# Optimization experiments

Measured on AMD Instinct MI355X. Metric: run time of the kernel, lower is better.

Reference implementation:

```python
import jax, jax.numpy as jnp
import numpy as np

N_HEADS = 16
ROPE_BASE = 10000.0


def _rope_tables(T, head_dim, dtype):
    d2 = head_dim // 2
    inv_freq = 1.0 / (ROPE_BASE ** (jnp.arange(0, head_dim, 2, dtype=jnp.float32) / head_dim))
    t = jnp.arange(T, dtype=jnp.float32)
    freqs = jnp.outer(t, inv_freq)  # [T, d2]
    cos = jnp.cos(freqs)[None, :, None, :].astype(dtype)  # [1,T,1,d2]
    sin = jnp.sin(freqs)[None, :, None, :].astype(dtype)
    return cos, sin


def _apply_rotary(x, cos, sin):
    # x: [B,T,H,D]; rotate halves
    d = x.shape[-1] // 2
    x1, x2 = x[..., :d], x[..., d:]
    return jnp.concatenate([x1 * cos + x2 * sin, -x1 * sin + x2 * cos], axis=-1)


def setup_inputs() -> dict:
    key = jax.random.key(0)
    k1, k2, k3 = jax.random.split(key, 3)
    B, T, C = 2, 2048, 1024
    x = jax.random.normal(k1, (B, T, C), dtype=jnp.float32)
    w_attn = jax.random.normal(k2, (3 * C, C), dtype=jnp.float32) * (1.0 / np.sqrt(C))
    w_proj = jax.random.normal(k3, (C, C), dtype=jnp.float32) * (1.0 / np.sqrt(C))
    return {"x": x, "w_attn": w_attn, "w_proj": w_proj}


def reference(x, w_attn, w_proj):
    B, T, C = x.shape
    H = N_HEADS
    D = C // H
    qkv = jnp.einsum('btc,fc->btf', x, w_attn)  # [B,T,3C]
    q, k, v = jnp.split(qkv, 3, axis=2)
    q = q.reshape(B, T, H, D)
    k = k.reshape(B, T, H, D)
    v = v.reshape(B, T, H, D)
    cos, sin = _rope_tables(T, D, x.dtype)
    q = _apply_rotary(q, cos, sin)
    k = _apply_rotary(k, cos, sin)
    # causal SDPA, scale 1/sqrt(D)
    scale = 1.0 / np.sqrt(D)
    scores = jnp.einsum('bqhd,bkhd->bhqk', q, k) * scale
    causal = jnp.tril(jnp.ones((T, T), dtype=bool))
    scores = jnp.where(causal[None, None], scores, jnp.finfo(scores.dtype).min)
    attn = jax.nn.softmax(scores, axis=-1)
    y = jnp.einsum('bhqk,bkhd->bqhd', attn, v).reshape(B, T, C)
    return jnp.einsum('btc,oc->bto', y, w_proj)
```

## Files before the change

### kernel.cpp

```cpp
#include <hip/hip_runtime.h>
#include <math.h>

typedef __bf16 bf16x8 __attribute__((ext_vector_type(8)));
typedef float f32x4 __attribute__((ext_vector_type(4)));

__device__ __forceinline__ unsigned f2bf(float f) {
    union { float f; unsigned u; } v; v.f = f;
    return (v.u + 0x7FFFu + ((v.u >> 16) & 1u)) >> 16;
}

__device__ __forceinline__ void gload16(const ushort* g, ushort* l) {
    __builtin_amdgcn_global_load_lds(
        (const __attribute__((address_space(1))) void*)g,
        (__attribute__((address_space(3))) void*)l, 16, 0, 0);
}

__device__ __forceinline__ bool src_is_fp32(const unsigned* s) {
    int sane = 0;
#pragma unroll
    for (int i = 0; i < 64; ++i) {
        unsigned lo = s[i] & 0xFFFFu;
        unsigned e = (lo >> 7) & 0xFF;
        if (lo == 0u || (e >= 100u && e <= 140u)) sane++;
    }
    return sane < 48;
}

__global__ __launch_bounds__(256) void tobf16_all_kernel(
    const unsigned* __restrict__ s0, const unsigned* __restrict__ s1,
    const unsigned* __restrict__ s2,
    ushort* __restrict__ d0, ushort* __restrict__ d1, ushort* __restrict__ d2) {
    const int bx = blockIdx.x;
    const unsigned* src;
    ushort* dst;
    int lb;
    if (bx < 2048)      { src = s0; dst = d0; lb = bx; }
    else if (bx < 3584) { src = s1; dst = d1; lb = bx - 2048; }
    else                { src = s2; dst = d2; lb = bx - 3584; }
    const int i = lb * 2048 + threadIdx.x * 8;
    if (src_is_fp32(src)) {
        const float* fs = (const float*)src;
        float4 f0 = *(const float4*)(fs + i);
        float4 f1 = *(const float4*)(fs + i + 4);
        uint4 o;
        o.x = f2bf(f0.x) | (f2bf(f0.y) << 16);
        o.y = f2bf(f0.z) | (f2bf(f0.w) << 16);
        o.z = f2bf(f1.x) | (f2bf(f1.y) << 16);
        o.w = f2bf(f1.z) | (f2bf(f1.w) << 16);
        *(uint4*)(dst + i) = o;
    } else {
        *(uint4*)(dst + i) = *(const uint4*)((const ushort*)src + i);
    }
}

constexpr int GBM = 128, GBN = 128, GBK = 32;

__global__ __launch_bounds__(256) void gemm_qkv_rope_kernel(
    const ushort* __restrict__ A, const ushort* __restrict__ Bmat,
    ushort* __restrict__ qkvh, int K) {
    __shared__ ushort As[GBM * GBK];
    __shared__ ushort Bs[GBN * GBK];

    const int tid  = threadIdx.x;
    const int lane = tid & 63;
    const int wv   = tid >> 6;
    const int wm   = (wv >> 1) * 64;
    const int wn   = (wv & 1) * 64;

    const ushort* Ab = A + (size_t)blockIdx.x * GBM * K;
    const ushort* Bb = Bmat + (size_t)blockIdx.y * GBN * K;

    f32x4 acc[4][4];
#pragma unroll
    for (int i = 0; i < 4; i++)
#pragma unroll
        for (int j = 0; j < 4; j++) acc[i][j] = (f32x4){0.f, 0.f, 0.f, 0.f};

    const int srow = tid >> 2;
    const int scol = (tid & 3) * 8;
    const int fr = lane & 15;
    const int fk = (lane >> 4) * 8;
    ushort* adst = As + wv * 512;
    ushort* bdst = Bs + wv * 512;

    for (int k0 = 0; k0 < K; k0 += GBK) {
        __syncthreads();
        gload16(Ab + (size_t)srow * K + k0 + scol,        adst);
        gload16(Ab + (size_t)(srow + 64) * K + k0 + scol, adst + 2048);
        gload16(Bb + (size_t)srow * K + k0 + scol,        bdst);
        gload16(Bb + (size_t)(srow + 64) * K + k0 + scol, bdst + 2048);
        __syncthreads();

        bf16x8 af[4], bfr[4];
#pragma unroll
        for (int i = 0; i < 4; i++)
            af[i] = *(const bf16x8*)(As + (wm + i * 16 + fr) * GBK + fk);
#pragma unroll
        for (int j = 0; j < 4; j++)
            bfr[j] = *(const bf16x8*)(Bs + (wn + j * 16 + fr) * GBK + fk);
#pragma unroll
        for (int i = 0; i < 4; i++)
#pragma unroll
            for (int j = 0; j < 4; j++)
                acc[i][j] = __builtin_amdgcn_mfma_f32_16x16x32_bf16(af[i], bfr[j], acc[i][j], 0, 0, 0);
    }

    const int crow0 = (lane >> 4) * 4;
    const int col0  = blockIdx.y * GBN + wn;
    const int which = col0 >> 10;
    const int hh    = (col0 >> 6) & 15;
    ushort* outp = qkvh + (size_t)which * 4194304 + (size_t)hh * 131072;

    if (which < 2) {
        const float inva = exp2f((float)fr * -0.41524101186f);
        const float invb = exp2f((float)(fr + 16) * -0.41524101186f);
        const float qs = (which == 0) ? 0.125f : 1.0f;
#pragma unroll
        for (int i = 0; i < 4; i++)
#pragma unroll
            for (int r = 0; r < 4; r++) {
                int row = blockIdx.x * GBM + wm + i * 16 + crow0 + r;
                int t = row & 2047;
                size_t ob = ((size_t)(row >> 11)) * 2097152 + (size_t)t * 64;
                float sa, ca, sb, cb;
                __sincosf((float)t * inva, &sa, &ca);
                __sincosf((float)t * invb, &sb, &cb);
                float q0 = acc[i][0][r], q1 = acc[i][1][r];
                float q2 = acc[i][2][r], q3 = acc[i][3][r];
                float n0 = (q0 * ca + q2 * sa) * qs;
                float n1 = (q1 * cb + q3 * sb) * qs;
                float n2 = (q2 * ca - q0 * sa) * qs;
                float n3 = (q3 * cb - q1 * sb) * qs;
                outp[ob + fr]      = (ushort)f2bf(n0);
                outp[ob + 16 + fr] = (ushort)f2bf(n1);
                outp[ob + 32 + fr] = (ushort)f2bf(n2);
                outp[ob + 48 + fr] = (ushort)f2bf(n3);
            }
    } else {
#pragma unroll
        for (int i = 0; i < 4; i++)
#pragma unroll
            for (int r = 0; r < 4; r++) {
                int row = blockIdx.x * GBM + wm + i * 16 + crow0 + r;
                int t = row & 2047;
                size_t ob = ((size_t)(row >> 11)) * 2097152 + (size_t)t * 64;
#pragma unroll
                for (int j = 0; j < 4; j++)
                    outp[ob + j * 16 + fr] = (ushort)f2bf(acc[i][j][r]);
            }
    }
}

__global__ __launch_bounds__(256) void gemm_bt_kernel(
    const ushort* __restrict__ A, const ushort* __restrict__ Bmat,
    float* __restrict__ C, int M, int N, int K) {
    __shared__ ushort As[GBM * GBK];
    __shared__ ushort Bs[GBN * GBK];

    const int tid  = threadIdx.x;
    const int lane = tid & 63;
    const int wv   = tid >> 6;
    const int wm   = (wv >> 1) * 64;
    const int wn   = (wv & 1) * 64;

    const ushort* Ab = A + (size_t)blockIdx.x * GBM * K;
    const ushort* Bb = Bmat + (size_t)blockIdx.y * GBN * K;

    f32x4 acc[4][4];
#pragma unroll
    for (int i = 0; i < 4; i++)
#pragma unroll
        for (int j = 0; j < 4; j++) acc[i][j] = (f32x4){0.f, 0.f, 0.f, 0.f};

    const int srow = tid >> 2;
    const int scol = (tid & 3) * 8;
    const int fr = lane & 15;
    const int fk = (lane >> 4) * 8;
    ushort* adst = As + wv * 512;
    ushort* bdst = Bs + wv * 512;

    for (int k0 = 0; k0 < K; k0 += GBK) {
        __syncthreads();
        gload16(Ab + (size_t)srow * K + k0 + scol,        adst);
        gload16(Ab + (size_t)(srow + 64) * K + k0 + scol, adst + 2048);
        gload16(Bb + (size_t)srow * K + k0 + scol,        bdst);
        gload16(Bb + (size_t)(srow + 64) * K + k0 + scol, bdst + 2048);
        __syncthreads();

        bf16x8 af[4], bfr[4];
#pragma unroll
        for (int i = 0; i < 4; i++)
            af[i] = *(const bf16x8*)(As + (wm + i * 16 + fr) * GBK + fk);
#pragma unroll
        for (int j = 0; j < 4; j++)
            bfr[j] = *(const bf16x8*)(Bs + (wn + j * 16 + fr) * GBK + fk);
#pragma unroll
        for (int i = 0; i < 4; i++)
#pragma unroll
            for (int j = 0; j < 4; j++)
                acc[i][j] = __builtin_amdgcn_mfma_f32_16x16x32_bf16(af[i], bfr[j], acc[i][j], 0, 0, 0);
    }

    const int crow0 = (lane >> 4) * 4;
#pragma unroll
    for (int i = 0; i < 4; i++)
#pragma unroll
        for (int j = 0; j < 4; j++)
#pragma unroll
            for (int r = 0; r < 4; r++) {
                int row = blockIdx.x * GBM + wm + i * 16 + crow0 + r;
                int col = blockIdx.y * GBN + wn + j * 16 + fr;
                C[(size_t)row * N + col] = acc[i][j][r];
            }
}

#define NEG_BIG (-1e30f)
constexpr int LPK = 72;
constexpr int LPV = 136;

__global__ __launch_bounds__(256) void attn_kernel(const ushort* __restrict__ qkvh,
                                                   ushort* __restrict__ y) {
    __shared__ ushort Ks[128 * LPK];
    __shared__ ushort Vt[64 * LPV];
    __shared__ ushort Ps[4][16 * LPV];

    const int tid  = threadIdx.x;
    const int lane = tid & 63;
    const int wv   = tid >> 6;
    const int pid  = blockIdx.x;
    const int bh   = blockIdx.y;
    const int b    = bh >> 4, h = bh & 15;

    const ushort* qp = qkvh + (size_t)b * 2097152 + (size_t)h * 131072;
    const ushort* kp = qp + 4194304;
    const ushort* vp = qp + 8388608;

    const int fr = lane & 15;
    const int fq = lane >> 4;
    const int fk = fq * 8;

    const int srow = tid >> 1;
    const int scol = (tid & 1) * 32;
    const int vkey = tid & 127;
    const int vd0  = (tid >> 7) * 32;

#pragma unroll 1
    for (int seg = 0; seg < 2; ++seg) {
        const int qb = seg ? (31 - pid) : pid;
        const int nIt = (qb + 2) >> 1;

        const int qrow = qb * 64 + wv * 16 + fr;
        bf16x8 qf0 = *(const bf16x8*)(qp + (size_t)qrow * 64 + fk);
        bf16x8 qf1 = *(const bf16x8*)(qp + (size_t)qrow * 64 + 32 + fk);

        f32x4 o[4];
        o[0] = o[1] = o[2] = o[3] = (f32x4){0.f, 0.f, 0.f, 0.f};
        float lacc[4] = {0.f, 0.f, 0.f, 0.f};

        uint4 kr0, kr1, kr2, kr3, vr0, vr1, vr2, vr3;
        {
            const ushort* sk = kp + (size_t)srow * 64 + scol;
            kr0 = *(const uint4*)(sk);
            kr1 = *(const uint4*)(sk + 8);
            kr2 = *(const uint4*)(sk + 16);
            kr3 = *(const uint4*)(sk + 24);
            const ushort* sv = vp + (size_t)vkey * 64 + vd0;
            vr0 = *(const uint4*)(sv);
            vr1 = *(const uint4*)(sv + 8);
            vr2 = *(const uint4*)(sv + 16);
            vr3 = *(const uint4*)(sv + 24);
        }

#pragma unroll 1
        for (int it = 0; it < nIt; ++it) {
            const int k0 = it * 128;
            __syncthreads();
            *(uint4*)(Ks + srow * LPK + scol)      = kr0;
            *(uint4*)(Ks + srow * LPK + scol + 8)  = kr1;
            *(uint4*)(Ks + srow * LPK + scol + 16) = kr2;
            *(uint4*)(Ks + srow * LPK + scol + 24) = kr3;
            {
                unsigned w[16] = {vr0.x, vr0.y, vr0.z, vr0.w, vr1.x, vr1.y, vr1.z, vr1.w,
                                  vr2.x, vr2.y, vr2.z, vr2.w, vr3.x, vr3.y, vr3.z, vr3.w};
#pragma unroll
                for (int jj = 0; jj < 16; ++jj) {
                    Vt[(vd0 + 2 * jj)     * LPV + vkey] = (ushort)(w[jj] & 0xFFFFu);
                    Vt[(vd0 + 2 * jj + 1) * LPV + vkey] = (ushort)(w[jj] >> 16);
                }
            }
            __syncthreads();
            if (it + 1 < nIt) {
                const ushort* sk = kp + (size_t)(k0 + 128 + srow) * 64 + scol;
                kr0 = *(const uint4*)(sk);
                kr1 = *(const uint4*)(sk + 8);
                kr2 = *(const uint4*)(sk + 16);
                kr3 = *(const uint4*)(sk + 24);
                const ushort* sv = vp + (size_t)(k0 + 128 + vkey) * 64 + vd0;
                vr0 = *(const uint4*)(sv);
                vr1 = *(const uint4*)(sv + 8);
                vr2 = *(const uint4*)(sv + 16);
                vr3 = *(const uint4*)(sv + 24);
            }

            f32x4 s[8];
#pragma unroll
            for (int j = 0; j < 8; ++j) {
                bf16x8 kf0 = *(const bf16x8*)(Ks + (j * 16 + fr) * LPK + fk);
                bf16x8 kf1 = *(const bf16x8*)(Ks + (j * 16 + fr) * LPK + 32 + fk);
                f32x4 z = (f32x4){0.f, 0.f, 0.f, 0.f};
                z = __builtin_amdgcn_mfma_f32_16x16x32_bf16(qf0, kf0, z, 0, 0, 0);
                z = __builtin_amdgcn_mfma_f32_16x16x32_bf16(qf1, kf1, z, 0, 0, 0);
                s[j] = z;
            }
            if (it + 1 < nIt) {
#pragma unroll
                for (int j = 0; j < 8; ++j)
#pragma unroll
                    for (int r = 0; r < 4; ++r) {
                        float p = __expf(s[j][r]);
                        s[j][r] = p;
                        lacc[r] += p;
                    }
            } else {
                const int rowg = qb * 64 + wv * 16 + fq * 4;
#pragma unroll
                for (int j = 0; j < 8; ++j)
#pragma unroll
                    for (int r = 0; r < 4; ++r) {
                        float v = s[j][r];
                        if ((k0 + j * 16 + fr) > (rowg + r)) v = NEG_BIG;
                        float p = __expf(v);
                        s[j][r] = p;
                        lacc[r] += p;
                    }
            }

            ushort* pw = Ps[wv];
#pragma unroll
            for (int j = 0; j < 8; ++j)
#pragma unroll
                for (int r = 0; r < 4; ++r)
                    pw[(fq * 4 + r) * LPV + j * 16 + fr] = (ushort)f2bf(s[j][r]);
            __asm__ volatile("" ::: "memory");

#pragma unroll
            for (int kk = 0; kk < 4; ++kk) {
                bf16x8 pf = *(const bf16x8*)(pw + fr * LPV + kk * 32 + fk);
#pragma unroll
                for (int j = 0; j < 4; ++j) {
                    bf16x8 vf = *(const bf16x8*)(Vt + (j * 16 + fr) * LPV + kk * 32 + fk);
                    o[j] = __builtin_amdgcn_mfma_f32_16x16x32_bf16(pf, vf, o[j], 0, 0, 0);
                }
            }
        }

#pragma unroll
        for (int msk = 1; msk < 16; msk <<= 1)
#pragma unroll
            for (int r = 0; r < 4; ++r)
                lacc[r] += __shfl_xor(lacc[r], msk, 64);
#pragma unroll
        for (int j = 0; j < 4; ++j)
#pragma unroll
            for (int r = 0; r < 4; ++r) {
                int row = qb * 64 + wv * 16 + fq * 4 + r;
                y[((size_t)b * 2048 + row) * 1024 + h * 64 + j * 16 + fr] =
                    (ushort)f2bf(o[j][r] / lacc[r]);
            }
    }
}

extern "C" void kernel_launch(void* const* d_in, const int* in_sizes, int n_in,
                              void* d_out, int out_size, void* d_ws, size_t ws_size,
                              hipStream_t stream) {
    const int nx = in_sizes[0];
    const int na = in_sizes[1];
    const int np = in_sizes[2];

    ushort* qkvh = (ushort*)d_ws;
    ushort* yb   = qkvh + (size_t)3 * 4194304;
    ushort* xb   = yb + (size_t)4096 * 1024;
    ushort* wab  = xb + nx;
    ushort* wpb  = wab + na;
    size_t need = ((size_t)3 * 4194304 + (size_t)4096 * 1024 + nx + na + np) * 2;
    if (ws_size < need) return;

    tobf16_all_kernel<<<dim3(4096), 256, 0, stream>>>(
        (const unsigned*)d_in[0], (const unsigned*)d_in[1], (const unsigned*)d_in[2],
        xb, wab, wpb);

    gemm_qkv_rope_kernel<<<dim3(32, 24), 256, 0, stream>>>(xb, wab, qkvh, 1024);
    attn_kernel<<<dim3(16, 32), 256, 0, stream>>>(qkvh, yb);
    gemm_bt_kernel<<<dim3(32, 8), 256, 0, stream>>>(yb, wpb, (float*)d_out, 4096, 1024, 1024);
}
```

Baseline: 204.9 us.

## Double-buffer LDS tiles in GEMMs and attention with smaller key blocks

```diff
diff --git a/kernel.cpp b/kernel.cpp
--- a/kernel.cpp
+++ b/kernel.cpp
@@ -58,8 +58,8 @@
 __global__ __launch_bounds__(256) void gemm_qkv_rope_kernel(
     const ushort* __restrict__ A, const ushort* __restrict__ Bmat,
     ushort* __restrict__ qkvh, int K) {
-    __shared__ ushort As[GBM * GBK];
-    __shared__ ushort Bs[GBN * GBK];
+    __shared__ ushort As[2][GBM * GBK];
+    __shared__ ushort Bs[2][GBN * GBK];
 
     const int tid  = threadIdx.x;
     const int lane = tid & 63;
@@ -80,24 +80,31 @@
     const int scol = (tid & 3) * 8;
     const int fr = lane & 15;
     const int fk = (lane >> 4) * 8;
-    ushort* adst = As + wv * 512;
-    ushort* bdst = Bs + wv * 512;
-
-    for (int k0 = 0; k0 < K; k0 += GBK) {
+    const int nK = K >> 5;
+
+    gload16(Ab + (size_t)srow * K + scol,        As[0] + wv * 512);
+    gload16(Ab + (size_t)(srow + 64) * K + scol, As[0] + wv * 512 + 2048);
+    gload16(Bb + (size_t)srow * K + scol,        Bs[0] + wv * 512);
+    gload16(Bb + (size_t)(srow + 64) * K + scol, Bs[0] + wv * 512 + 2048);
+
+#pragma unroll 1
+    for (int it = 0; it < nK; ++it) {
+        const int cur = it & 1;
         __syncthreads();
-        gload16(Ab + (size_t)srow * K + k0 + scol,        adst);
-        gload16(Ab + (size_t)(srow + 64) * K + k0 + scol, adst + 2048);
-        gload16(Bb + (size_t)srow * K + k0 + scol,        bdst);
-        gload16(Bb + (size_t)(srow + 64) * K + k0 + scol, bdst + 2048);
-        __syncthreads();
-
+        if (it + 1 < nK) {
+            const int k0 = (it + 1) << 5, nxt = cur ^ 1;
+            gload16(Ab + (size_t)srow * K + k0 + scol,        As[nxt] + wv * 512);
+            gload16(Ab + (size_t)(srow + 64) * K + k0 + scol, As[nxt] + wv * 512 + 2048);
+            gload16(Bb + (size_t)srow * K + k0 + scol,        Bs[nxt] + wv * 512);
+            gload16(Bb + (size_t)(srow + 64) * K + k0 + scol, Bs[nxt] + wv * 512 + 2048);
+        }
         bf16x8 af[4], bfr[4];
 #pragma unroll
         for (int i = 0; i < 4; i++)
-            af[i] = *(const bf16x8*)(As + (wm + i * 16 + fr) * GBK + fk);
+            af[i] = *(const bf16x8*)(As[cur] + (wm + i * 16 + fr) * GBK + fk);
 #pragma unroll
         for (int j = 0; j < 4; j++)
-            bfr[j] = *(const bf16x8*)(Bs + (wn + j * 16 + fr) * GBK + fk);
+            bfr[j] = *(const bf16x8*)(Bs[cur] + (wn + j * 16 + fr) * GBK + fk);
 #pragma unroll
         for (int i = 0; i < 4; i++)
 #pragma unroll
@@ -154,8 +161,8 @@
 __global__ __launch_bounds__(256) void gemm_bt_kernel(
     const ushort* __restrict__ A, const ushort* __restrict__ Bmat,
     float* __restrict__ C, int M, int N, int K) {
-    __shared__ ushort As[GBM * GBK];
-    __shared__ ushort Bs[GBN * GBK];
+    __shared__ ushort As[2][GBM * GBK];
+    __shared__ ushort Bs[2][GBN * GBK];
 
     const int tid  = threadIdx.x;
     const int lane = tid & 63;
@@ -176,24 +183,31 @@
     const int scol = (tid & 3) * 8;
     const int fr = lane & 15;
     const int fk = (lane >> 4) * 8;
-    ushort* adst = As + wv * 512;
-    ushort* bdst = Bs + wv * 512;
-
-    for (int k0 = 0; k0 < K; k0 += GBK) {
+    const int nK = K >> 5;
+
+    gload16(Ab + (size_t)srow * K + scol,        As[0] + wv * 512);
+    gload16(Ab + (size_t)(srow + 64) * K + scol, As[0] + wv * 512 + 2048);
+    gload16(Bb + (size_t)srow * K + scol,        Bs[0] + wv * 512);
+    gload16(Bb + (size_t)(srow + 64) * K + scol, Bs[0] + wv * 512 + 2048);
+
+#pragma unroll 1
+    for (int it = 0; it < nK; ++it) {
+        const int cur = it & 1;
         __syncthreads();
-        gload16(Ab + (size_t)srow * K + k0 + scol,        adst);
-        gload16(Ab + (size_t)(srow + 64) * K + k0 + scol, adst + 2048);
-        gload16(Bb + (size_t)srow * K + k0 + scol,        bdst);
-        gload16(Bb + (size_t)(srow + 64) * K + k0 + scol, bdst + 2048);
-        __syncthreads();
-
+        if (it + 1 < nK) {
+            const int k0 = (it + 1) << 5, nxt = cur ^ 1;
+            gload16(Ab + (size_t)srow * K + k0 + scol,        As[nxt] + wv * 512);
+            gload16(Ab + (size_t)(srow + 64) * K + k0 + scol, As[nxt] + wv * 512 + 2048);
+            gload16(Bb + (size_t)srow * K + k0 + scol,        Bs[nxt] + wv * 512);
+            gload16(Bb + (size_t)(srow + 64) * K + k0 + scol, Bs[nxt] + wv * 512 + 2048);
+        }
         bf16x8 af[4], bfr[4];
 #pragma unroll
         for (int i = 0; i < 4; i++)
-            af[i] = *(const bf16x8*)(As + (wm + i * 16 + fr) * GBK + fk);
+            af[i] = *(const bf16x8*)(As[cur] + (wm + i * 16 + fr) * GBK + fk);
 #pragma unroll
         for (int j = 0; j < 4; j++)
-            bfr[j] = *(const bf16x8*)(Bs + (wn + j * 16 + fr) * GBK + fk);
+            bfr[j] = *(const bf16x8*)(Bs[cur] + (wn + j * 16 + fr) * GBK + fk);
 #pragma unroll
         for (int i = 0; i < 4; i++)
 #pragma unroll
@@ -215,14 +229,13 @@
 }
 
 #define NEG_BIG (-1e30f)
-constexpr int LPK = 72;
-constexpr int LPV = 136;
+constexpr int LP = 72;
 
 __global__ __launch_bounds__(256) void attn_kernel(const ushort* __restrict__ qkvh,
                                                    ushort* __restrict__ y) {
-    __shared__ ushort Ks[128 * LPK];
-    __shared__ ushort Vt[64 * LPV];
-    __shared__ ushort Ps[4][16 * LPV];
+    __shared__ ushort Ks[2][64 * LP];
+    __shared__ ushort Vt[2][64 * LP];
+    __shared__ ushort Ps[4][16 * LP];
 
     const int tid  = threadIdx.x;
     const int lane = tid & 63;
@@ -239,15 +252,17 @@
     const int fq = lane >> 4;
     const int fk = fq * 8;
 
-    const int srow = tid >> 1;
-    const int scol = (tid & 1) * 32;
-    const int vkey = tid & 127;
-    const int vd0  = (tid >> 7) * 32;
+    const int krow = tid >> 2;
+    const int kcol = (tid & 3) * 16;
+    const int vkey = tid & 63;
+    const int vd0  = (tid >> 6) * 16;
 
 #pragma unroll 1
     for (int seg = 0; seg < 2; ++seg) {
         const int qb = seg ? (31 - pid) : pid;
-        const int nIt = (qb + 2) >> 1;
+        const int nIt = qb + 1;
+
+        __syncthreads();
 
         const int qrow = qb * 64 + wv * 16 + fr;
         bf16x8 qf0 = *(const bf16x8*)(qp + (size_t)qrow * 64 + fk);
@@ -257,56 +272,62 @@
         o[0] = o[1] = o[2] = o[3] = (f32x4){0.f, 0.f, 0.f, 0.f};
         float lacc[4] = {0.f, 0.f, 0.f, 0.f};
 
-        uint4 kr0, kr1, kr2, kr3, vr0, vr1, vr2, vr3;
+        uint4 kr0, kr1, vr0, vr1;
         {
-            const ushort* sk = kp + (size_t)srow * 64 + scol;
+            const ushort* sk = kp + (size_t)krow * 64 + kcol;
             kr0 = *(const uint4*)(sk);
             kr1 = *(const uint4*)(sk + 8);
-            kr2 = *(const uint4*)(sk + 16);
-            kr3 = *(const uint4*)(sk + 24);
             const ushort* sv = vp + (size_t)vkey * 64 + vd0;
             vr0 = *(const uint4*)(sv);
             vr1 = *(const uint4*)(sv + 8);
-            vr2 = *(const uint4*)(sv + 16);
-            vr3 = *(const uint4*)(sv + 24);
+            *(uint4*)(Ks[0] + krow * LP + kcol)     = kr0;
+            *(uint4*)(Ks[0] + krow * LP + kcol + 8) = kr1;
+            unsigned w[8] = {vr0.x, vr0.y, vr0.z, vr0.w, vr1.x, vr1.y, vr1.z, vr1.w};
+#pragma unroll
+            for (int jj = 0; jj < 8; ++jj) {
+                Vt[0][(vd0 + 2 * jj)     * LP + vkey] = (ushort)(w[jj] & 0xFFFFu);
+                Vt[0][(vd0 + 2 * jj + 1) * LP + vkey] = (ushort)(w[jj] >> 16);
+            }
+        }
+        if (1 < nIt) {
+            const ushort* sk = kp + (size_t)(64 + krow) * 64 + kcol;
+            kr0 = *(const uint4*)(sk);
+            kr1 = *(const uint4*)(sk + 8);
+            const ushort* sv = vp + (size_t)(64 + vkey) * 64 + vd0;
+            vr0 = *(const uint4*)(sv);
+            vr1 = *(const uint4*)(sv + 8);
         }
 
 #pragma unroll 1
         for (int it = 0; it < nIt; ++it) {
-            const int k0 = it * 128;
-            __syncthreads();
-            *(uint4*)(Ks + srow * LPK + scol)      = kr0;
-            *(uint4*)(Ks + srow * LPK + scol + 8)  = kr1;
-            *(uint4*)(Ks + srow * LPK + scol + 16) = kr2;
-            *(uint4*)(Ks + srow * LPK + scol + 24) = kr3;
-            {
-                unsigned w[16] = {vr0.x, vr0.y, vr0.z, vr0.w, vr1.x, vr1.y, vr1.z, vr1.w,
-                                  vr2.x, vr2.y, vr2.z, vr2.w, vr3.x, vr3.y, vr3.z, vr3.w};
-#pragma unroll
-                for (int jj = 0; jj < 16; ++jj) {
-                    Vt[(vd0 + 2 * jj)     * LPV + vkey] = (ushort)(w[jj] & 0xFFFFu);
-                    Vt[(vd0 + 2 * jj + 1) * LPV + vkey] = (ushort)(w[jj] >> 16);
-                }
-            }
+            const int cur = it & 1;
+            const int k0 = it * 64;
             __syncthreads();
             if (it + 1 < nIt) {
-                const ushort* sk = kp + (size_t)(k0 + 128 + srow) * 64 + scol;
-                kr0 = *(const uint4*)(sk);
-                kr1 = *(const uint4*)(sk + 8);
-                kr2 = *(const uint4*)(sk + 16);
-                kr3 = *(const uint4*)(sk + 24);
-                const ushort* sv = vp + (size_t)(k0 + 128 + vkey) * 64 + vd0;
-                vr0 = *(const uint4*)(sv);
-                vr1 = *(const uint4*)(sv + 8);
-                vr2 = *(const uint4*)(sv + 16);
-                vr3 = *(const uint4*)(sv + 24);
-            }
-
-            f32x4 s[8];
-#pragma unroll
-            for (int j = 0; j < 8; ++j) {
-                bf16x8 kf0 = *(const bf16x8*)(Ks + (j * 16 + fr) * LPK + fk);
-                bf16x8 kf1 = *(const bf16x8*)(Ks + (j * 16 + fr) * LPK + 32 + fk);
+                const int nxt = cur ^ 1;
+                *(uint4*)(Ks[nxt] + krow * LP + kcol)     = kr0;
+                *(uint4*)(Ks[nxt] + krow * LP + kcol + 8) = kr1;
+                unsigned w[8] = {vr0.x, vr0.y, vr0.z, vr0.w, vr1.x, vr1.y, vr1.z, vr1.w};
+#pragma unroll
+                for (int jj = 0; jj < 8; ++jj) {
+                    Vt[nxt][(vd0 + 2 * jj)     * LP + vkey] = (ushort)(w[jj] & 0xFFFFu);
+                    Vt[nxt][(vd0 + 2 * jj + 1) * LP + vkey] = (ushort)(w[jj] >> 16);
+                }
+                if (it + 2 < nIt) {
+                    const ushort* sk = kp + (size_t)(k0 + 128 + krow) * 64 + kcol;
+                    kr0 = *(const uint4*)(sk);
+                    kr1 = *(const uint4*)(sk + 8);
+                    const ushort* sv = vp + (size_t)(k0 + 128 + vkey) * 64 + vd0;
+                    vr0 = *(const uint4*)(sv);
+                    vr1 = *(const uint4*)(sv + 8);
+                }
+            }
+
+            f32x4 s[4];
+#pragma unroll
+            for (int j = 0; j < 4; ++j) {
+                bf16x8 kf0 = *(const bf16x8*)(Ks[cur] + (j * 16 + fr) * LP + fk);
+                bf16x8 kf1 = *(const bf16x8*)(Ks[cur] + (j * 16 + fr) * LP + 32 + fk);
                 f32x4 z = (f32x4){0.f, 0.f, 0.f, 0.f};
                 z = __builtin_amdgcn_mfma_f32_16x16x32_bf16(qf0, kf0, z, 0, 0, 0);
                 z = __builtin_amdgcn_mfma_f32_16x16x32_bf16(qf1, kf1, z, 0, 0, 0);
@@ -314,7 +335,7 @@
             }
             if (it + 1 < nIt) {
 #pragma unroll
-                for (int j = 0; j < 8; ++j)
+                for (int j = 0; j < 4; ++j)
 #pragma unroll
                     for (int r = 0; r < 4; ++r) {
                         float p = __expf(s[j][r]);
@@ -324,7 +345,7 @@
             } else {
                 const int rowg = qb * 64 + wv * 16 + fq * 4;
 #pragma unroll
-                for (int j = 0; j < 8; ++j)
+                for (int j = 0; j < 4; ++j)
 #pragma unroll
                     for (int r = 0; r < 4; ++r) {
                         float v = s[j][r];
@@ -337,18 +358,18 @@
 
             ushort* pw = Ps[wv];
 #pragma unroll
-            for (int j = 0; j < 8; ++j)
+            for (int j = 0; j < 4; ++j)
 #pragma unroll
                 for (int r = 0; r < 4; ++r)
-                    pw[(fq * 4 + r) * LPV + j * 16 + fr] = (ushort)f2bf(s[j][r]);
+                    pw[(fq * 4 + r) * LP + j * 16 + fr] = (ushort)f2bf(s[j][r]);
             __asm__ volatile("" ::: "memory");
 
 #pragma unroll
-            for (int kk = 0; kk < 4; ++kk) {
-                bf16x8 pf = *(const bf16x8*)(pw + fr * LPV + kk * 32 + fk);
+            for (int kk = 0; kk < 2; ++kk) {
+                bf16x8 pf = *(const bf16x8*)(pw + fr * LP + kk * 32 + fk);
 #pragma unroll
                 for (int j = 0; j < 4; ++j) {
-                    bf16x8 vf = *(const bf16x8*)(Vt + (j * 16 + fr) * LPV + kk * 32 + fk);
+                    bf16x8 vf = *(const bf16x8*)(Vt[cur] + (j * 16 + fr) * LP + kk * 32 + fk);
                     o[j] = __builtin_amdgcn_mfma_f32_16x16x32_bf16(pf, vf, o[j], 0, 0, 0);
                 }
             }
```

Result: no change. 201.5 us (-1.7%).
